# Kernel optimization log

Measured on AMD Instinct MI355X. Metric: run time of the kernel, lower is better.

Reference implementation:

```python
import jax, jax.numpy as jnp
import numpy as np

B, S, H, NH = 2, 2048, 1024, 16
HD = H // NH
DFF = 4 * H
EPS = 1e-6


def layer_norm(x, g, b):
    mu = jnp.mean(x, axis=-1, keepdims=True)
    var = jnp.mean(jnp.square(x - mu), axis=-1, keepdims=True)
    return (x - mu) * jax.lax.rsqrt(var + EPS) * g + b


def setup_inputs() -> dict:
    key = jax.random.key(0)
    ks = jax.random.split(key, 10)
    s = 0.02
    return {
        "x": jax.random.normal(ks[0], (B, S, H), jnp.float32),
        "attention_mask": jnp.triu(jnp.ones((S, S), jnp.bool_), k=1),  # causal: True = masked
        "ln1_g": jnp.ones((H,), jnp.float32),
        "ln1_b": jnp.zeros((H,), jnp.float32),
        "ln2_g": jnp.ones((H,), jnp.float32),
        "ln2_b": jnp.zeros((H,), jnp.float32),
        "qkv_w": jax.random.normal(ks[1], (3 * H, H), jnp.float32) * s,
        "out_w": jax.random.normal(ks[2], (H, H), jnp.float32) * s,
        "fc1_w": jax.random.normal(ks[3], (DFF, H), jnp.float32) * s,
        "fc1_b": jnp.zeros((DFF,), jnp.float32),
        "fc2_w": jax.random.normal(ks[4], (H, DFF), jnp.float32) * s,
        "fc2_b": jnp.zeros((H,), jnp.float32),
    }


def reference(x, attention_mask, ln1_g, ln1_b, ln2_g, ln2_b,
              qkv_w, out_w, fc1_w, fc1_b, fc2_w, fc2_b):
    scale = HD ** -0.5
    # --- attention sub-block (pre-norm) ---
    residual = x
    h = layer_norm(x, ln1_g, ln1_b)
    qkv = h @ qkv_w.T                              # [B,S,3H]
    q, k, v = jnp.split(qkv, 3, axis=-1)
    def heads(t):                                  # [B,S,H] -> [B,NH,S,HD]
        return t.reshape(B, S, NH, HD).transpose(0, 2, 1, 3)
    q, k, v = heads(q), heads(k), heads(v)
    scores = jnp.einsum('bhqd,bhkd->bhqk', q, k) * scale
    scores = jnp.where(attention_mask[None, None, :, :], -jnp.inf, scores)
    attn = jax.nn.softmax(scores, axis=-1)
    attn = jnp.nan_to_num(attn, nan=0.0, posinf=0.0, neginf=0.0)
    ctx = jnp.einsum('bhqk,bhkd->bhqd', attn, v)
    ctx = ctx.transpose(0, 2, 1, 3).reshape(B, S, H)
    x = residual + ctx @ out_w.T
    # --- MLP sub-block (pre-norm) ---
    residual = x
    h = layer_norm(x, ln2_g, ln2_b)
    h = jax.nn.gelu(h @ fc1_w.T + fc1_b, approximate=False)
    x = residual + h @ fc2_w.T + fc2_b
    return x
```

## Files before the change

kernel.cpp:

```cpp
#include <hip/hip_runtime.h>
#include <hip/hip_bf16.h>
#include <math.h>

#define B_   2
#define S_   2048
#define H_   1024
#define NH_  16
#define HD_  64
#define DFF_ 4096
#define ROWS (B_*S_)
#define EPS_ 1e-6f
#define NQT  (S_/64)

typedef __hip_bfloat16 bf16;
typedef __attribute__((ext_vector_type(8))) short s8;
typedef __attribute__((ext_vector_type(4))) float f32x4;

__device__ __forceinline__ bf16 to_bf16(float f) { return __float2bfloat16(f); }

#define GLOAD_LDS16(g, l) __builtin_amdgcn_global_load_lds( \
    (const __attribute__((address_space(1))) void*)(g),     \
    (__attribute__((address_space(3))) void*)(l), 16, 0, 0)

__global__ __launch_bounds__(256) void cast_all(const float* __restrict__ w0,
                                                const float* __restrict__ w1,
                                                const float* __restrict__ w2,
                                                const float* __restrict__ w3,
                                                bf16* __restrict__ o0, bf16* __restrict__ o1,
                                                bf16* __restrict__ o2, bf16* __restrict__ o3) {
    size_t u = (size_t)blockIdx.x * 256 + threadIdx.x;
    const size_t n0 = (size_t)3*H_*H_/8, n1 = (size_t)H_*H_/8, n2 = (size_t)DFF_*H_/8;
    const float* src; bf16* dst; size_t base;
    if (u < n0)              { src = w0; dst = o0; base = u; }
    else if (u < n0+n1)      { src = w1; dst = o1; base = u-n0; }
    else if (u < n0+n1+n2)   { src = w2; dst = o2; base = u-n0-n1; }
    else                     { src = w3; dst = o3; base = u-n0-n1-n2; }
    size_t i = base * 8;
    float4 a = *reinterpret_cast<const float4*>(src + i);
    float4 b = *reinterpret_cast<const float4*>(src + i + 4);
    union { bf16 h[8]; s8 v; } uu;
    uu.h[0]=to_bf16(a.x); uu.h[1]=to_bf16(a.y); uu.h[2]=to_bf16(a.z); uu.h[3]=to_bf16(a.w);
    uu.h[4]=to_bf16(b.x); uu.h[5]=to_bf16(b.y); uu.h[6]=to_bf16(b.z); uu.h[7]=to_bf16(b.w);
    *reinterpret_cast<s8*>(dst + i) = uu.v;
}

__global__ __launch_bounds__(256) void ln_bf16(const float* __restrict__ x,
                                               const float* __restrict__ g,
                                               const float* __restrict__ b,
                                               bf16* __restrict__ y) {
    int row = blockIdx.x;
    int t = threadIdx.x;
    float4 v = reinterpret_cast<const float4*>(x + (size_t)row * H_)[t];
    float s  = v.x + v.y + v.z + v.w;
    float ss = v.x*v.x + v.y*v.y + v.z*v.z + v.w*v.w;
    #pragma unroll
    for (int m = 1; m < 64; m <<= 1) {
        s  += __shfl_xor(s,  m, 64);
        ss += __shfl_xor(ss, m, 64);
    }
    __shared__ float ws_s[4], ws_ss[4];
    int wid = t >> 6;
    if ((t & 63) == 0) { ws_s[wid] = s; ws_ss[wid] = ss; }
    __syncthreads();
    s  = ws_s[0] + ws_s[1] + ws_s[2] + ws_s[3];
    ss = ws_ss[0] + ws_ss[1] + ws_ss[2] + ws_ss[3];
    float mu   = s * (1.0f / H_);
    float var  = ss * (1.0f / H_) - mu * mu;
    float rstd = rsqrtf(var + EPS_);
    float4 gv = reinterpret_cast<const float4*>(g)[t];
    float4 bv = reinterpret_cast<const float4*>(b)[t];
    union { bf16 h[4]; short4 sv; } u;
    u.h[0] = to_bf16((v.x - mu) * rstd * gv.x + bv.x);
    u.h[1] = to_bf16((v.y - mu) * rstd * gv.y + bv.y);
    u.h[2] = to_bf16((v.z - mu) * rstd * gv.z + bv.z);
    u.h[3] = to_bf16((v.w - mu) * rstd * gv.w + bv.w);
    *reinterpret_cast<short4*>(y + (size_t)row * H_ + t * 4) = u.sv;
}

template<int EPI, int TN, int OCC, int DB>
__global__ __launch_bounds__(256, OCC) void gemm_bf16(const bf16* __restrict__ A,
                                                      const bf16* __restrict__ Bw,
                                                      bf16* __restrict__ Cb,
                                                      float* __restrict__ Cf,
                                                      bf16* __restrict__ vT,
                                                      const float* __restrict__ bias,
                                                      const float* __restrict__ res,
                                                      int M, int N, int K, int GX) {
    const int NJ = TN / 32;
    const int LA = 128 * 64, LB = TN * 64;
    __shared__ bf16 As[DB * LA];
    __shared__ bf16 Bs[DB * LB];

    int nwg = gridDim.x;
    int ld  = blockIdx.x;
    int wgid = (ld & 7) * (nwg >> 3) + (ld >> 3);
    int by = wgid / GX, bx = wgid % GX;

    int t = threadIdx.x, l = t & 63, w = t >> 6;
    int lr = l & 15, lg = l >> 4;
    size_t bm = (size_t)by * 128, bn = (size_t)bx * TN;

    int sx = lr & 7;
    int scol = ((t & 7) ^ ((t >> 3) & 7)) * 8;
    const bf16* Ag = A  + (bm + (t >> 3)) * K + scol;
    const bf16* Bg = Bw + (bn + (t >> 3)) * K + scol;

    int wr = (w >> 1) << 6, wc = (w & 1) * (TN / 2);

    f32x4 acc[4][NJ];
    const f32x4 z4 = {0.f, 0.f, 0.f, 0.f};
    #pragma unroll
    for (int i = 0; i < 4; ++i)
        #pragma unroll
        for (int j = 0; j < NJ; ++j) acc[i][j] = z4;

    auto STAGE = [&](int buf, int k0) {
        #pragma unroll
        for (int c = 0; c < 4; ++c)
            GLOAD_LDS16(Ag + k0 + (size_t)c * 32 * K, As + buf * LA + w * 512 + c * 2048);
        #pragma unroll
        for (int c = 0; c < NJ; ++c)
            GLOAD_LDS16(Bg + k0 + (size_t)c * 32 * K, Bs + buf * LB + w * 512 + c * 2048);
    };

    auto COMPUTE = [&](int buf) {
        const bf16* Ab = As + buf * LA;
        const bf16* Bb = Bs + buf * LB;
        #pragma unroll
        for (int kk = 0; kk < 64; kk += 32) {
            s8 af[4], bfr[NJ];
            #pragma unroll
            for (int i = 0; i < 4; ++i)
                af[i] = *reinterpret_cast<const s8*>(Ab + (wr + i*16 + lr) * 64
                                                        + ((((kk >> 3) + lg) ^ sx) * 8));
            #pragma unroll
            for (int j = 0; j < NJ; ++j)
                bfr[j] = *reinterpret_cast<const s8*>(Bb + (wc + j*16 + lr) * 64
                                                         + ((((kk >> 3) + lg) ^ sx) * 8));
            #pragma unroll
            for (int i = 0; i < 4; ++i)
                #pragma unroll
                for (int j = 0; j < NJ; ++j)
                    acc[i][j] = __builtin_amdgcn_mfma_f32_16x16x32_bf16(af[i], bfr[j], acc[i][j], 0, 0, 0);
        }
    };

    if (DB == 1) {
        for (int k0 = 0; k0 < K; k0 += 64) {
            STAGE(0, k0);
            asm volatile("s_waitcnt vmcnt(0)" ::: "memory");
            __syncthreads();
            COMPUTE(0);
            __syncthreads();
        }
    } else {
        const int NT = K >> 6;
        STAGE(0, 0);
        asm volatile("s_waitcnt vmcnt(0)" ::: "memory");
        __syncthreads();
        int cur = 0;
        for (int it = 0; it < NT; ++it) {
            if (it + 1 < NT) STAGE(cur ^ 1, (it + 1) << 6);
            COMPUTE(cur);
            asm volatile("s_waitcnt vmcnt(0)" ::: "memory");
            __syncthreads();
            cur ^= 1;
        }
    }

    float bias_v[NJ];
    if (EPI == 2 || EPI == 3) {
        #pragma unroll
        for (int j = 0; j < NJ; ++j) bias_v[j] = bias[bn + wc + j*16 + lr];
    }
    #pragma unroll
    for (int i = 0; i < 4; ++i) {
        #pragma unroll
        for (int q = 0; q < 4; ++q) {
            size_t rg = bm + wr + i*16 + lg*4 + q;
            #pragma unroll
            for (int j = 0; j < NJ; ++j) {
                size_t cg = bn + wc + j*16 + lr;
                float v = acc[i][j][q];
                if (EPI == 0) {
                    if (cg < 2048) {
                        Cb[rg * N + cg] = to_bf16(v);
                    } else {
                        int hd = (int)cg - 2048;
                        int hh = hd >> 6, d = hd & 63;
                        int bb = (int)(rg >> 11), sq = (int)(rg & 2047);
                        vT[(((size_t)(bb * NH_ + hh)) * HD_ + d) * S_ + sq] = to_bf16(v);
                    }
                } else if (EPI == 1) {
                    Cf[rg * N + cg] = v + res[rg * N + cg];
                } else if (EPI == 2) {
                    float u = v + bias_v[j];
                    u = 0.5f * u * (1.0f + erff(u * 0.70710678118654752f));
                    Cb[rg * N + cg] = to_bf16(u);
                } else {
                    Cf[rg * N + cg] = v + bias_v[j] + res[rg * N + cg];
                }
            }
        }
    }
}

__global__ __launch_bounds__(512, 2) void gemm256_fc1(const bf16* __restrict__ A,
                                                      const bf16* __restrict__ Bw,
                                                      bf16* __restrict__ C,
                                                      const float* __restrict__ bias,
                                                      int M, int N, int K) {
    __shared__ bf16 As[2][256 * 64];
    __shared__ bf16 Bs[2][256 * 64];

    int nwg = gridDim.x;
    int ld  = blockIdx.x;
    int wgid = (ld & 7) * (nwg >> 3) + (ld >> 3);
    int GX = N >> 8;
    int by = wgid / GX, bx = wgid % GX;
    size_t bm = (size_t)by << 8, bn = (size_t)bx << 8;

    int t = threadIdx.x, l = t & 63, w = t >> 6;
    int lr = l & 15, lg = l >> 4;
    int wr2 = w >> 2, wc2 = w & 3;
    int sx = lr & 7;

    int scol = ((l & 7) ^ (l >> 3)) * 8;
    const bf16* Ag = A  + (bm + w * 8 + (l >> 3)) * K + scol;
    const bf16* Bg = Bw + (bn + w * 8 + (l >> 3)) * K + scol;

    f32x4 acc[8][4];
    const f32x4 z4 = {0.f, 0.f, 0.f, 0.f};
    #pragma unroll
    for (int i = 0; i < 8; ++i)
        #pragma unroll
        for (int j = 0; j < 4; ++j) acc[i][j] = z4;

    auto STAGE = [&](int buf, int k0) {
        #pragma unroll
        for (int s = 0; s < 4; ++s)
            GLOAD_LDS16(Ag + k0 + (size_t)s * 64 * K, &As[buf][s * 4096 + w * 512]);
        #pragma unroll
        for (int s = 0; s < 4; ++s)
            GLOAD_LDS16(Bg + k0 + (size_t)s * 64 * K, &Bs[buf][s * 4096 + w * 512]);
    };

    auto KSLICE = [&](int buf, int kx) {
        s8 af[8], bfr[4];
        #pragma unroll
        for (int m4 = 0; m4 < 8; ++m4) {
            int R = wr2 * 128 + m4 * 16 + lr;
            af[m4] = *reinterpret_cast<const s8*>(&As[buf][R * 64 + (((kx << 2) + lg) ^ sx) * 8]);
        }
        #pragma unroll
        for (int n2 = 0; n2 < 4; ++n2) {
            int R = wc2 * 64 + n2 * 16 + lr;
            bfr[n2] = *reinterpret_cast<const s8*>(&Bs[buf][R * 64 + (((kx << 2) + lg) ^ sx) * 8]);
        }
        __builtin_amdgcn_s_setprio(1);
        #pragma unroll
        for (int m4 = 0; m4 < 8; ++m4)
            #pragma unroll
            for (int n2 = 0; n2 < 4; ++n2)
                acc[m4][n2] = __builtin_amdgcn_mfma_f32_16x16x32_bf16(af[m4], bfr[n2],
                                                                      acc[m4][n2], 0, 0, 0);
        __builtin_amdgcn_s_setprio(0);
        __builtin_amdgcn_sched_barrier(0);
    };

    const int NT = K >> 6;
    STAGE(0, 0);
    STAGE(1, 64);
    for (int tt = 0; tt < NT; ++tt) {
        int buf = tt & 1;
        if (tt + 1 < NT) { asm volatile("s_waitcnt vmcnt(8)" ::: "memory"); }
        else             { asm volatile("s_waitcnt vmcnt(0)" ::: "memory"); }
        __builtin_amdgcn_s_barrier();
        KSLICE(buf, 0);
        KSLICE(buf, 1);
        __builtin_amdgcn_s_barrier();
        if (tt + 2 < NT) STAGE(buf, (tt + 2) << 6);
    }

    float bv[4];
    int colb = (int)bn + wc2 * 64;
    #pragma unroll
    for (int n = 0; n < 4; ++n) bv[n] = bias[colb + n * 16 + lr];
    #pragma unroll
    for (int m = 0; m < 8; ++m) {
        #pragma unroll
        for (int q = 0; q < 4; ++q) {
            size_t rg = bm + wr2 * 128 + m * 16 + lg * 4 + q;
            #pragma unroll
            for (int n = 0; n < 4; ++n) {
                float u = acc[m][n][q] + bv[n];
                u = 0.5f * u * (1.0f + erff(u * 0.70710678118654752f));
                C[rg * N + colb + n * 16 + lr] = to_bf16(u);
            }
        }
    }
}

#define KVB 128

__device__ __forceinline__ s8 scale_q8(s8 v) {
    union { s8 v; bf16 h[8]; } u; u.v = v;
    #pragma unroll
    for (int e = 0; e < 8; ++e)
        u.h[e] = to_bf16(__bfloat162float(u.h[e]) * 0.125f);
    return u.v;
}

__device__ __forceinline__ void attn_qtile(int qt, int h, int b, int t,
                                           const bf16* __restrict__ qkvb,
                                           const bf16* __restrict__ vT,
                                           bf16* __restrict__ ctx,
                                           bf16* Ks, bf16* Vt, bf16* Pw) {
    int l = t & 63, w = t >> 6, lr = l & 15, lg = l >> 4;
    int qb = qt * 64;

    const bf16* qp = qkvb + ((size_t)(b * S_) + qb + w * 16 + lr) * (3 * H_) + h * HD_;
    s8 qf0 = scale_q8(*reinterpret_cast<const s8*>(qp + lg * 8));
    s8 qf1 = scale_q8(*reinterpret_cast<const s8*>(qp + 32 + lg * 8));

    const f32x4 z4 = {0.f, 0.f, 0.f, 0.f};
    f32x4 oacc[4];
    #pragma unroll
    for (int n = 0; n < 4; ++n) oacc[n] = z4;
    float lsum[4] = {0.f, 0.f, 0.f, 0.f};

    int krow = t >> 1, kcol = (t & 1) * 32;
    int vd   = t >> 2, vk = (t & 3) * 8;
    const bf16* kbase = qkvb + ((size_t)(b * S_) + krow) * (3 * H_) + H_ + h * HD_ + kcol;
    const bf16* vbase = vT + ((size_t)((b * NH_ + h) * HD_) + vd) * S_ + vk;

    int nt = (qt >> 1) + 1;
    s8 k0 = *reinterpret_cast<const s8*>(kbase);
    s8 k1 = *reinterpret_cast<const s8*>(kbase + 8);
    s8 k2 = *reinterpret_cast<const s8*>(kbase + 16);
    s8 k3 = *reinterpret_cast<const s8*>(kbase + 24);
    s8 v0 = *reinterpret_cast<const s8*>(vbase);
    s8 v1 = *reinterpret_cast<const s8*>(vbase + 32);
    s8 v2 = *reinterpret_cast<const s8*>(vbase + 64);
    s8 v3 = *reinterpret_cast<const s8*>(vbase + 96);

    for (int it = 0; it < nt; ++it) {
        int kvb0 = it * KVB;
        __syncthreads();
        *reinterpret_cast<s8*>(&Ks[krow * 72 + kcol])      = k0;
        *reinterpret_cast<s8*>(&Ks[krow * 72 + kcol + 8])  = k1;
        *reinterpret_cast<s8*>(&Ks[krow * 72 + kcol + 16]) = k2;
        *reinterpret_cast<s8*>(&Ks[krow * 72 + kcol + 24]) = k3;
        *reinterpret_cast<s8*>(&Vt[vd * 136 + vk])         = v0;
        *reinterpret_cast<s8*>(&Vt[vd * 136 + vk + 32])    = v1;
        *reinterpret_cast<s8*>(&Vt[vd * 136 + vk + 64])    = v2;
        *reinterpret_cast<s8*>(&Vt[vd * 136 + vk + 96])    = v3;
        int nx = (it + 1 < nt) ? kvb0 + KVB : kvb0;
        const bf16* kn = kbase + (size_t)nx * (3 * H_);
        const bf16* vn = vbase + nx;
        k0 = *reinterpret_cast<const s8*>(kn);
        k1 = *reinterpret_cast<const s8*>(kn + 8);
        k2 = *reinterpret_cast<const s8*>(kn + 16);
        k3 = *reinterpret_cast<const s8*>(kn + 24);
        v0 = *reinterpret_cast<const s8*>(vn);
        v1 = *reinterpret_cast<const s8*>(vn + 32);
        v2 = *reinterpret_cast<const s8*>(vn + 64);
        v3 = *reinterpret_cast<const s8*>(vn + 96);
        __syncthreads();

        f32x4 sa[8];
        __builtin_amdgcn_s_setprio(1);
        #pragma unroll
        for (int n = 0; n < 8; ++n) {
            f32x4 zz = z4;
            s8 kf0 = *reinterpret_cast<const s8*>(&Ks[(n*16 + lr) * 72 + lg * 8]);
            s8 kf1 = *reinterpret_cast<const s8*>(&Ks[(n*16 + lr) * 72 + 32 + lg * 8]);
            zz = __builtin_amdgcn_mfma_f32_16x16x32_bf16(qf0, kf0, zz, 0, 0, 0);
            zz = __builtin_amdgcn_mfma_f32_16x16x32_bf16(qf1, kf1, zz, 0, 0, 0);
            sa[n] = zz;
        }
        __builtin_amdgcn_s_setprio(0);

        bool mask = (kvb0 + KVB > qb);
        #pragma unroll
        for (int q = 0; q < 4; ++q) {
            int qrow = qb + w*16 + lg*4 + q;
            #pragma unroll
            for (int n = 0; n < 8; ++n) {
                float s = sa[n][q];
                if (mask) {
                    int col = kvb0 + n*16 + lr;
                    s = (col <= qrow) ? s : -1e30f;
                }
                float e = __expf(s);
                lsum[q] += e;
                Pw[(lg*4 + q) * 136 + n*16 + lr] = to_bf16(e);
            }
        }
        asm volatile("s_waitcnt lgkmcnt(0)" ::: "memory");
        __builtin_amdgcn_sched_barrier(0);

        __builtin_amdgcn_s_setprio(1);
        #pragma unroll
        for (int ks = 0; ks < 4; ++ks) {
            s8 pf = *reinterpret_cast<const s8*>(&Pw[lr * 136 + ks*32 + lg * 8]);
            #pragma unroll
            for (int n = 0; n < 4; ++n) {
                s8 vf = *reinterpret_cast<const s8*>(&Vt[(n*16 + lr) * 136 + ks*32 + lg * 8]);
                oacc[n] = __builtin_amdgcn_mfma_f32_16x16x32_bf16(pf, vf, oacc[n], 0, 0, 0);
            }
        }
        __builtin_amdgcn_s_setprio(0);
    }

    #pragma unroll
    for (int m = 1; m < 16; m <<= 1) {
        #pragma unroll
        for (int q = 0; q < 4; ++q) lsum[q] += __shfl_xor(lsum[q], m, 64);
    }

    #pragma unroll
    for (int q = 0; q < 4; ++q) {
        float inv = 1.0f / lsum[q];
        size_t row = (size_t)(b * S_) + qb + w * 16 + lg * 4 + q;
        #pragma unroll
        for (int n = 0; n < 4; ++n)
            ctx[row * H_ + h * HD_ + n * 16 + lr] = to_bf16(oacc[n][q] * inv);
    }
}

__global__ __launch_bounds__(256) void attn_mfma(const bf16* __restrict__ qkvb,
                                                 const bf16* __restrict__ vT,
                                                 bf16* __restrict__ ctx) {
    __shared__ bf16 Ks[KVB * 72];
    __shared__ bf16 Vt[64 * 136];
    __shared__ bf16 Pw[4][16 * 136];
    int h = blockIdx.y, b = blockIdx.z, t = threadIdx.x;
    int w = t >> 6;
    attn_qtile(blockIdx.x,           h, b, t, qkvb, vT, ctx, Ks, Vt, Pw[w]);
    attn_qtile(NQT - 1 - blockIdx.x, h, b, t, qkvb, vT, ctx, Ks, Vt, Pw[w]);
}

extern "C" void kernel_launch(void* const* d_in, const int* in_sizes, int n_in,
                              void* d_out, int out_size, void* d_ws, size_t ws_size,
                              hipStream_t stream) {
    const float* x     = (const float*)d_in[0];
    const float* ln1_g = (const float*)d_in[2];
    const float* ln1_b = (const float*)d_in[3];
    const float* ln2_g = (const float*)d_in[4];
    const float* ln2_b = (const float*)d_in[5];
    const float* qkv_w = (const float*)d_in[6];
    const float* out_w = (const float*)d_in[7];
    const float* fc1_w = (const float*)d_in[8];
    const float* fc1_b = (const float*)d_in[9];
    const float* fc2_w = (const float*)d_in[10];
    const float* fc2_b = (const float*)d_in[11];
    float* out = (float*)d_out;

    bf16* w_qkv  = (bf16*)d_ws;
    bf16* w_out  = w_qkv  + (size_t)3*H_*H_;
    bf16* w_fc1  = w_out  + (size_t)H_*H_;
    bf16* w_fc2  = w_fc1  + (size_t)DFF_*H_;
    bf16* h_bf   = w_fc2  + (size_t)H_*DFF_;
    bf16* qkv_bf = h_bf   + (size_t)ROWS*H_;
    bf16* vTb    = qkv_bf + (size_t)ROWS*3*H_;
    bf16* ctx_bf = vTb    + (size_t)B_*NH_*HD_*S_;
    bf16* ff_bf  = ctx_bf + (size_t)ROWS*H_;

    cast_all<<<6144, 256, 0, stream>>>(qkv_w, out_w, fc1_w, fc2_w,
                                       w_qkv, w_out, w_fc1, w_fc2);

    ln_bf16<<<ROWS, 256, 0, stream>>>(x, ln1_g, ln1_b, h_bf);
    gemm_bf16<0,128,2,1><<<32 * 24, 256, 0, stream>>>(h_bf, w_qkv, qkv_bf, nullptr, vTb,
                                                      nullptr, nullptr, ROWS, 3*H_, H_, 24);
    attn_mfma<<<dim3(NQT/2, NH_, B_), 256, 0, stream>>>(qkv_bf, vTb, ctx_bf);
    gemm_bf16<1,64,3,2><<<32 * 16, 256, 0, stream>>>(ctx_bf, w_out, nullptr, out, nullptr,
                                                     nullptr, x, ROWS, H_, H_, 16);
    ln_bf16<<<ROWS, 256, 0, stream>>>(out, ln2_g, ln2_b, h_bf);
    gemm256_fc1<<<256, 512, 0, stream>>>(h_bf, w_fc1, ff_bf, fc1_b, ROWS, DFF_, H_);
    gemm_bf16<3,64,3,2><<<32 * 16, 256, 0, stream>>>(ff_bf, w_fc2, nullptr, out, nullptr,
                                                     fc2_b, out, ROWS, H_, DFF_, 16);
}
```

Baseline: 234.7 us.

## Split fc1 GEMM K-tile into half-slices with finer-grained load/compute interleave

The fc1 GEMM shared-memory tiles are split into two 32-wide K halves with a new swizzle, and each iteration is broken into four MFMA phases. Global-to-LDS loads for upcoming half-tiles are issued between these phases, and the B fragment reads are halved to lower register pressure. The goal is to hide load latency more smoothly and cut the stall at the single per-tile barrier. The cost is many more barriers and lgkmcnt waits per tile, which could serialize the waves.

```diff
diff --git a/kernel.cpp b/kernel.cpp
--- a/kernel.cpp
+++ b/kernel.cpp
@@ -210,8 +210,8 @@
                                                       bf16* __restrict__ C,
                                                       const float* __restrict__ bias,
                                                       int M, int N, int K) {
-    __shared__ bf16 As[2][256 * 64];
-    __shared__ bf16 Bs[2][256 * 64];
+    __shared__ bf16 As[2][2][256 * 32];
+    __shared__ bf16 Bs[2][2][256 * 32];
 
     int nwg = gridDim.x;
     int ld  = blockIdx.x;
@@ -223,11 +223,11 @@
     int t = threadIdx.x, l = t & 63, w = t >> 6;
     int lr = l & 15, lg = l >> 4;
     int wr2 = w >> 2, wc2 = w & 3;
-    int sx = lr & 7;
-
-    int scol = ((l & 7) ^ (l >> 3)) * 8;
-    const bf16* Ag = A  + (bm + w * 8 + (l >> 3)) * K + scol;
-    const bf16* Bg = Bw + (bn + w * 8 + (l >> 3)) * K + scol;
+    int rsw = (lr & 3) ^ ((lr >> 2) & 3);
+
+    int ssw = (((t & 3) ^ ((t >> 2) & 3) ^ ((t >> 4) & 3))) * 8;
+    const bf16* Asrc = A  + (bm + w * 16 + (l >> 2)) * K + ssw;
+    const bf16* Bsrc = Bw + (bn + w * 16 + (l >> 2)) * K + ssw;
 
     f32x4 acc[8][4];
     const f32x4 z4 = {0.f, 0.f, 0.f, 0.f};
@@ -236,50 +236,87 @@
         #pragma unroll
         for (int j = 0; j < 4; ++j) acc[i][j] = z4;
 
-    auto STAGE = [&](int buf, int k0) {
-        #pragma unroll
-        for (int s = 0; s < 4; ++s)
-            GLOAD_LDS16(Ag + k0 + (size_t)s * 64 * K, &As[buf][s * 4096 + w * 512]);
-        #pragma unroll
-        for (int s = 0; s < 4; ++s)
-            GLOAD_LDS16(Bg + k0 + (size_t)s * 64 * K, &Bs[buf][s * 4096 + w * 512]);
-    };
-
-    auto KSLICE = [&](int buf, int kx) {
-        s8 af[8], bfr[4];
+    auto STG_A = [&](int x, int kh) {
+        int buf = x & 1, k0 = x << 6;
+        #pragma unroll
+        for (int j = 0; j < 2; ++j)
+            GLOAD_LDS16(Asrc + (size_t)j * 128 * K + k0 + kh * 32,
+                        &As[buf][kh][j * 4096 + w * 512]);
+    };
+    auto STG_B = [&](int x, int kh) {
+        int buf = x & 1, k0 = x << 6;
+        #pragma unroll
+        for (int j = 0; j < 2; ++j)
+            GLOAD_LDS16(Bsrc + (size_t)j * 128 * K + k0 + kh * 32,
+                        &Bs[buf][kh][j * 4096 + w * 512]);
+    };
+
+    s8 af[8], bfr[2];
+    auto RD_A = [&](int buf, int kx) {
         #pragma unroll
         for (int m4 = 0; m4 < 8; ++m4) {
             int R = wr2 * 128 + m4 * 16 + lr;
-            af[m4] = *reinterpret_cast<const s8*>(&As[buf][R * 64 + (((kx << 2) + lg) ^ sx) * 8]);
-        }
-        #pragma unroll
-        for (int n2 = 0; n2 < 4; ++n2) {
-            int R = wc2 * 64 + n2 * 16 + lr;
-            bfr[n2] = *reinterpret_cast<const s8*>(&Bs[buf][R * 64 + (((kx << 2) + lg) ^ sx) * 8]);
-        }
+            af[m4] = *reinterpret_cast<const s8*>(&As[buf][kx][R * 32 + (lg ^ rsw) * 8]);
+        }
+    };
+    auto RD_B = [&](int buf, int kx, int nh) {
+        #pragma unroll
+        for (int n2 = 0; n2 < 2; ++n2) {
+            int R = wc2 * 64 + (nh * 2 + n2) * 16 + lr;
+            bfr[n2] = *reinterpret_cast<const s8*>(&Bs[buf][kx][R * 32 + (lg ^ rsw) * 8]);
+        }
+    };
+    auto MFMA16 = [&](int nh) {
         __builtin_amdgcn_s_setprio(1);
         #pragma unroll
         for (int m4 = 0; m4 < 8; ++m4)
             #pragma unroll
-            for (int n2 = 0; n2 < 4; ++n2)
-                acc[m4][n2] = __builtin_amdgcn_mfma_f32_16x16x32_bf16(af[m4], bfr[n2],
-                                                                      acc[m4][n2], 0, 0, 0);
+            for (int n2 = 0; n2 < 2; ++n2)
+                acc[m4][nh*2 + n2] = __builtin_amdgcn_mfma_f32_16x16x32_bf16(
+                    af[m4], bfr[n2], acc[m4][nh*2 + n2], 0, 0, 0);
         __builtin_amdgcn_s_setprio(0);
-        __builtin_amdgcn_sched_barrier(0);
     };
 
     const int NT = K >> 6;
-    STAGE(0, 0);
-    STAGE(1, 64);
+    STG_A(0, 0); STG_B(0, 0); STG_A(0, 1); STG_B(0, 1);
+    STG_A(1, 0); STG_B(1, 0);
+    asm volatile("s_waitcnt vmcnt(4)" ::: "memory");
+    __builtin_amdgcn_s_barrier();
+
     for (int tt = 0; tt < NT; ++tt) {
         int buf = tt & 1;
-        if (tt + 1 < NT) { asm volatile("s_waitcnt vmcnt(8)" ::: "memory"); }
+        RD_A(buf, 0);
+        RD_B(buf, 0, 0);
+        if (tt + 1 < NT) STG_A(tt + 1, 1);
+        __builtin_amdgcn_s_barrier();
+        asm volatile("s_waitcnt lgkmcnt(0)" ::: "memory");
+        __builtin_amdgcn_sched_barrier(0);
+        MFMA16(0);
+        __builtin_amdgcn_s_barrier();
+        RD_B(buf, 0, 1);
+        if (tt + 1 < NT) STG_B(tt + 1, 1);
+        __builtin_amdgcn_s_barrier();
+        asm volatile("s_waitcnt lgkmcnt(0)" ::: "memory");
+        __builtin_amdgcn_sched_barrier(0);
+        MFMA16(1);
+        __builtin_amdgcn_s_barrier();
+        RD_A(buf, 1);
+        RD_B(buf, 1, 0);
+        if (tt + 2 < NT) STG_A(tt + 2, 0);
+        __builtin_amdgcn_s_barrier();
+        asm volatile("s_waitcnt lgkmcnt(0)" ::: "memory");
+        __builtin_amdgcn_sched_barrier(0);
+        MFMA16(0);
+        __builtin_amdgcn_s_barrier();
+        RD_B(buf, 1, 1);
+        if (tt + 2 < NT) STG_B(tt + 2, 0);
+        __builtin_amdgcn_s_barrier();
+        asm volatile("s_waitcnt lgkmcnt(0)" ::: "memory");
+        __builtin_amdgcn_sched_barrier(0);
+        MFMA16(1);
+        if (tt + 2 < NT) { asm volatile("s_waitcnt vmcnt(4)" ::: "memory"); }
         else             { asm volatile("s_waitcnt vmcnt(0)" ::: "memory"); }
         __builtin_amdgcn_s_barrier();
-        KSLICE(buf, 0);
-        KSLICE(buf, 1);
-        __builtin_amdgcn_s_barrier();
-        if (tt + 2 < NT) STAGE(buf, (tt + 2) << 6);
     }
 
     float bv[4];
```

After: 236.3 us. No clear change (+0.7%).
